# Optimization experiments

Hardware: AMD Instinct MI355X
Metric: run time of the kernel (lower is better)

The kernel has to match this reference:

```python
import jax, jax.numpy as jnp
import numpy as np

KEEP_P = 0.75  # 1 - dropout_p, dropout_p = 0.25

def setup_inputs() -> dict:
    key = jax.random.key(0)
    k1, k2, k3, k4 = jax.random.split(key, 4)
    B, Sq, Skv, D, Dv = 8, 2048, 2048, 128, 128
    x1 = jax.random.normal(k1, (B, Sq, D), dtype=jnp.float32)
    x2 = jax.random.normal(k2, (B, Skv, D), dtype=jnp.float32)
    x3 = jax.random.normal(k3, (B, Skv, Dv), dtype=jnp.float32)
    # torch Dropout(p): mask = bernoulli(keep_p) / keep_p
    keep = jax.random.bernoulli(k4, KEEP_P, (B, Sq, Skv))
    dropout_mask = keep.astype(jnp.float32) / KEEP_P
    return {"x1": x1, "x2": x2, "x3": x3, "dropout_mask": dropout_mask}

def reference(x1, x2, x3, dropout_mask):
    # scores: [B, Sq, Skv] = x1 @ x2^T (no scale: scale_factor is None)
    scores = jnp.einsum("bqd,bkd->bqk", x1, x2)
    probs = jax.nn.softmax(scores, axis=-1)
    probs = probs * dropout_mask  # dropout with fixed mask
    out = jnp.einsum("bqk,bkv->bqv", probs, x3)  # [B, Sq, Dv]
    return out
```

## Files before the change

### kernel.cpp

```cpp
#include <hip/hip_runtime.h>
#include <stdint.h>

#define SQ 2048
#define SKV 2048
#define DD 128
#define NB 8
#define M0 40.0f
#define KEEP_INV 1.3333333333333333f

typedef float  f4v  __attribute__((ext_vector_type(4)));
typedef __bf16 bf4  __attribute__((ext_vector_type(4)));
typedef __bf16 bf8  __attribute__((ext_vector_type(8)));

__device__ __forceinline__ void async16(const void* g, void* l) {
    __builtin_amdgcn_global_load_lds(
        (const __attribute__((address_space(1))) void*)g,
        (__attribute__((address_space(3))) void*)l, 16, 0, 0);
}

__device__ __forceinline__ f4v mfma16(bf8 a, bf8 b, f4v c) {
    return __builtin_amdgcn_mfma_f32_16x16x32_bf16(a, b, c, 0, 0, 0);
}

__global__ void cast_hilo_swz(const float* __restrict__ src,
                              __bf16* __restrict__ hi, __bf16* __restrict__ lo) {
    int tid = blockIdx.x * 256 + threadIdx.x;
    int d8 = tid & 15;
    int kv = (tid >> 4) & (SKV - 1);
    int b  = tid >> 15;
    const float* p = src + ((size_t)b * SKV + kv) * DD + d8 * 8;
    f4v a0 = *(const f4v*)p;
    f4v a1 = *(const f4v*)(p + 4);
    bf8 h, l;
#pragma unroll
    for (int c = 0; c < 4; c++) {
        __bf16 h0 = (__bf16)a0[c]; __bf16 h1 = (__bf16)a1[c];
        h[c] = h0; h[c + 4] = h1;
        l[c]     = (__bf16)(a0[c] - (float)h0);
        l[c + 4] = (__bf16)(a1[c] - (float)h1);
    }
    int s = d8 >> 2, g = d8 & 3, kb32 = kv >> 5, row = kv & 31;
    size_t off = (size_t)(b * 64 + kb32) * 4096 + (size_t)((s * 32 + row) * 4 + g) * 8;
    *(bf8*)(hi + off) = h;
    *(bf8*)(lo + off) = l;
}

__global__ void transpose_v_swz(const float* __restrict__ v, __bf16* __restrict__ vtf) {
    __shared__ __bf16 tile[32][33];
    int kb32 = blockIdx.x, dv0 = blockIdx.y * 32, b = blockIdx.z;
    int tx = threadIdx.x, ty = threadIdx.y;
    const float* src = v + ((size_t)b * SKV + kb32 * 32 + ty) * DD + dv0 + tx;
#pragma unroll
    for (int i = 0; i < 32; i += 8)
        tile[ty + i][tx] = (__bf16)src[(size_t)i * DD];
    __syncthreads();
    int pcol = (tx < 16) ? ((tx >> 2) << 3) + (tx & 3)
                         : (((tx - 16) >> 2) << 3) + 4 + (tx & 3);
    __bf16* dst = vtf + (size_t)(b * 64 + kb32) * 4096 + pcol;
#pragma unroll
    for (int i = 0; i < 32; i += 8)
        dst[(size_t)(dv0 + ty + i) * 32] = tile[tx][ty + i];
}

__global__ void maskbits_kernel(const float* __restrict__ mask,
                                uint32_t* __restrict__ bits) {
    int tid = blockIdx.x * 256 + threadIdx.x;
    const f4v* m = (const f4v*)(mask + (size_t)tid * 32);
    uint32_t w = 0;
#pragma unroll
    for (int c = 0; c < 8; c++) {
        f4v x = m[c];
        w |= (x.x > 0.5f ? 1u : 0u) << (c * 4);
        w |= (x.y > 0.5f ? 1u : 0u) << (c * 4 + 1);
        w |= (x.z > 0.5f ? 1u : 0u) << (c * 4 + 2);
        w |= (x.w > 0.5f ? 1u : 0u) << (c * 4 + 3);
    }
    bits[tid] = w;
}

__global__ __launch_bounds__(256, 3) void attn_kernel(
    const float* __restrict__ Qf, const __bf16* __restrict__ KV,
    const uint32_t* __restrict__ Mbits, __bf16* __restrict__ O_part,
    float* __restrict__ l_part, int nsp, int kv_len) {
    __shared__ __bf16 lds[2][12288];
    const int lin = blockIdx.x;
    const int per_xcd = (NB * nsp) >> 3;
    const int xcd = lin & 7;
    const int idx = lin >> 3;
    const int slice = xcd * per_xcd + (idx >> 5);
    const int qblk = idx & 31;
    const int b = slice / nsp, sid = slice % nsp;
    const int tid = threadIdx.x;
    const int w = tid >> 6, lane = tid & 63;
    const int g = lane >> 4, n = lane & 15;
    const int qb = qblk * 64 + w * 16;
    const int kb32_0 = (sid * kv_len) >> 5;
    const int niter = kv_len >> 5;
    const size_t kelems = (size_t)NB * SKV * DD;

    const float* Qrow = Qf + ((size_t)b * SQ + qb + n) * DD + g * 8;
    bf8 qh[4], ql[4];
#pragma unroll
    for (int s = 0; s < 4; s++) {
        f4v v0 = *(const f4v*)(Qrow + s * 32);
        f4v v1 = *(const f4v*)(Qrow + s * 32 + 4);
#pragma unroll
        for (int c = 0; c < 4; c++) {
            __bf16 h0 = (__bf16)v0[c];
            __bf16 h1 = (__bf16)v1[c];
            qh[s][c]     = h0;
            qh[s][c + 4] = h1;
            ql[s][c]     = (__bf16)(v0[c] - (float)h0);
            ql[s][c + 4] = (__bf16)(v1[c] - (float)h1);
        }
    }

    const __bf16* gblk0 = KV + (size_t)(b * 64 + kb32_0) * 4096;
    auto stage = [&](int buf, int it) {
        const __bf16* gb = gblk0 + (size_t)it * 4096;
#pragma unroll
        for (int jj = 0; jj < 6; jj++) {
            int j = w * 6 + jj;
            int arr = j >> 3, sub = j & 7;
            async16(gb + (size_t)arr * kelems + sub * 512 + lane * 8,
                    (void*)&lds[buf][arr * 4096 + sub * 512]);
        }
    };

    const uint32_t* Mrow = Mbits + ((size_t)b * SQ + qb + n) * (SKV / 32) + kb32_0;
    stage(0, 0);
    uint32_t mw_c = Mrow[0];
    uint32_t mw_n = (niter > 1) ? Mrow[1] : mw_c;

    const f4v zero = {0.f, 0.f, 0.f, 0.f};
    f4v o_acc[8];
#pragma unroll
    for (int t = 0; t < 8; t++) o_acc[t] = zero;
    float l_run = 0.f;

    for (int it = 0; it < niter; it++) {
        __syncthreads();
        if (it + 1 < niter) stage((it + 1) & 1, it + 1);
        uint32_t mw_p = Mrow[(it + 2 < niter) ? it + 2 : niter - 1];

        const __bf16* L = lds[it & 1];
        f4v sa0 = zero, sa1 = zero;
#pragma unroll
        for (int s = 0; s < 4; s++) {
            bf8 ah0 = *(const bf8*)(L + (size_t)((s * 32 + n) * 4 + g) * 8);
            bf8 ah1 = *(const bf8*)(L + (size_t)((s * 32 + n + 16) * 4 + g) * 8);
            bf8 al0 = *(const bf8*)(L + 4096 + (size_t)((s * 32 + n) * 4 + g) * 8);
            bf8 al1 = *(const bf8*)(L + 4096 + (size_t)((s * 32 + n + 16) * 4 + g) * 8);
            sa0 = mfma16(ah0, qh[s], sa0);
            sa1 = mfma16(ah1, qh[s], sa1);
            sa0 = mfma16(ah0, ql[s], sa0);
            sa1 = mfma16(ah1, ql[s], sa1);
            sa0 = mfma16(al0, qh[s], sa0);
            sa1 = mfma16(al1, qh[s], sa1);
        }

        float p0e[4], p1e[4];
#pragma unroll
        for (int r = 0; r < 4; r++) {
            p0e[r] = __expf(sa0[r] - M0);
            p1e[r] = __expf(sa1[r] - M0);
            l_run += p0e[r] + p1e[r];
        }
        bf8 pf;
#pragma unroll
        for (int j = 0; j < 4; j++) {
            pf[j]     = ((mw_c >> (4 * g + j)) & 1)      ? (__bf16)p0e[j] : (__bf16)0.0f;
            pf[j + 4] = ((mw_c >> (16 + 4 * g + j)) & 1) ? (__bf16)p1e[j] : (__bf16)0.0f;
        }
#pragma unroll
        for (int t = 0; t < 8; t++) {
            bf8 vf = *(const bf8*)(L + 8192 + (size_t)((t * 16 + n) * 4 + g) * 8);
            o_acc[t] = mfma16(pf, vf, o_acc[t]);
        }
        mw_c = mw_n; mw_n = mw_p;
    }

    l_run += __shfl_xor(l_run, 16);
    l_run += __shfl_xor(l_run, 32);
    const int tile = (b * 128 + qblk * 4 + w) * nsp + sid;
    __bf16* op = O_part + (size_t)tile * 2048;
#pragma unroll
    for (int t = 0; t < 8; t++)
#pragma unroll
        for (int r = 0; r < 4; r++)
            op[(g * 4 + r) * 128 + t * 16 + n] = (__bf16)o_acc[t][r];
    if (g == 0) l_part[(size_t)tile * 16 + n] = l_run;
}

__global__ __launch_bounds__(256) void combine_kernel(
    const __bf16* __restrict__ O_part, const float* __restrict__ l_part,
    float* __restrict__ out, int nsp) {
    const int qt = blockIdx.x;
    const int b  = blockIdx.y;
    const int tbase = (b * 128 + qt) * nsp;
    const int q  = threadIdx.x >> 4;
    const int d8 = threadIdx.x & 15;
    float acc[8] = {0.f, 0.f, 0.f, 0.f, 0.f, 0.f, 0.f, 0.f};
    float L = 0.f;
    for (int s = 0; s < nsp; s++) {
        const __bf16* op = O_part + (size_t)(tbase + s) * 2048 + q * 128 + d8 * 8;
        bf4 v0 = *(const bf4*)op;
        bf4 v1 = *(const bf4*)(op + 4);
#pragma unroll
        for (int e = 0; e < 4; e++) {
            acc[e]     += (float)v0[e];
            acc[e + 4] += (float)v1[e];
        }
        L += l_part[(size_t)(tbase + s) * 16 + q];
    }
    float scale = KEEP_INV / L;
    f4v w0, w1;
#pragma unroll
    for (int e = 0; e < 4; e++) { w0[e] = acc[e] * scale; w1[e] = acc[e + 4] * scale; }
    float* o = out + ((size_t)b * SQ + qt * 16 + q) * DD + d8 * 8;
    *(f4v*)o = w0;
    *(f4v*)(o + 4) = w1;
}

extern "C" void kernel_launch(void* const* d_in, const int* in_sizes, int n_in,
                              void* d_out, int out_size, void* d_ws, size_t ws_size,
                              hipStream_t stream) {
    const float* x1   = (const float*)d_in[0];
    const float* x2   = (const float*)d_in[1];
    const float* x3   = (const float*)d_in[2];
    const float* mask = (const float*)d_in[3];
    float* out = (float*)d_out;

    const size_t kelems = (size_t)NB * SKV * DD;
    __bf16*   Khif = (__bf16*)d_ws;
    __bf16*   Klof = Khif + kelems;
    __bf16*   VTf  = Klof + kelems;
    uint32_t* Mb   = (uint32_t*)(VTf + kelems);
    const size_t mwords = (size_t)NB * SQ * (SKV / 32);
    __bf16*   O_part = (__bf16*)(Mb + mwords);

    size_t base = 3 * kelems * sizeof(__bf16) + mwords * 4;
    size_t per  = (size_t)NB * 128 * (2048 * sizeof(__bf16) + 16 * 4);
    int nsp = 4;
    while (nsp > 1 && base + (size_t)nsp * per > ws_size) nsp >>= 1;
    float* l_part = (float*)(O_part + (size_t)NB * 128 * nsp * 2048);

    hipLaunchKernelGGL(cast_hilo_swz, dim3(NB * SKV * 16 / 256), dim3(256), 0, stream,
                       x2, Khif, Klof);
    hipLaunchKernelGGL(transpose_v_swz, dim3(SKV / 32, DD / 32, NB), dim3(32, 8), 0,
                       stream, x3, VTf);
    hipLaunchKernelGGL(maskbits_kernel, dim3(NB * SQ * 64 / 256), dim3(256), 0, stream,
                       mask, Mb);
    hipLaunchKernelGGL(attn_kernel, dim3(32 * NB * nsp), dim3(256), 0, stream,
                       x1, Khif, Mb, O_part, l_part, nsp, SKV / nsp);
    hipLaunchKernelGGL(combine_kernel, dim3(128, NB), dim3(256), 0, stream,
                       O_part, l_part, out, nsp);
}
```

Measured before the change: 264.9 us.

## Replace split-bf16 QK^T with single fp16 MFMA and fp32 partials

Drops the hi/lo bf16 split of Q and K, which cost three MFMAs per tile, in favour of a single fp16 cast and one f16 MFMA per tile. This cuts QK matrix work by three times and removes the K-low staging, shrinking LDS per stage and raising the occupancy hint to 4. Partial outputs are now stored in fp32 instead of bf16, adding write and read traffic in the combine step. The risk is accuracy: scores from unscaled dot products with D=128 may lose precision or overflow in fp16, while exp uses a fixed M0 offset.

```diff
diff --git a/kernel.cpp b/kernel.cpp
--- a/kernel.cpp
+++ b/kernel.cpp
@@ -8,9 +8,10 @@
 #define M0 40.0f
 #define KEEP_INV 1.3333333333333333f
 
-typedef float  f4v  __attribute__((ext_vector_type(4)));
-typedef __bf16 bf4  __attribute__((ext_vector_type(4)));
-typedef __bf16 bf8  __attribute__((ext_vector_type(8)));
+typedef float    f4v __attribute__((ext_vector_type(4)));
+typedef __bf16   bf4 __attribute__((ext_vector_type(4)));
+typedef __bf16   bf8 __attribute__((ext_vector_type(8)));
+typedef _Float16 h8  __attribute__((ext_vector_type(8)));
 
 __device__ __forceinline__ void async16(const void* g, void* l) {
     __builtin_amdgcn_global_load_lds(
@@ -18,12 +19,8 @@
         (__attribute__((address_space(3))) void*)l, 16, 0, 0);
 }
 
-__device__ __forceinline__ f4v mfma16(bf8 a, bf8 b, f4v c) {
-    return __builtin_amdgcn_mfma_f32_16x16x32_bf16(a, b, c, 0, 0, 0);
-}
-
-__global__ void cast_hilo_swz(const float* __restrict__ src,
-                              __bf16* __restrict__ hi, __bf16* __restrict__ lo) {
+__global__ void cast_f16_swz(const float* __restrict__ src,
+                             _Float16* __restrict__ dst) {
     int tid = blockIdx.x * 256 + threadIdx.x;
     int d8 = tid & 15;
     int kv = (tid >> 4) & (SKV - 1);
@@ -31,18 +28,14 @@
     const float* p = src + ((size_t)b * SKV + kv) * DD + d8 * 8;
     f4v a0 = *(const f4v*)p;
     f4v a1 = *(const f4v*)(p + 4);
-    bf8 h, l;
+    h8 h;
 #pragma unroll
     for (int c = 0; c < 4; c++) {
-        __bf16 h0 = (__bf16)a0[c]; __bf16 h1 = (__bf16)a1[c];
-        h[c] = h0; h[c + 4] = h1;
-        l[c]     = (__bf16)(a0[c] - (float)h0);
-        l[c + 4] = (__bf16)(a1[c] - (float)h1);
+        h[c]     = (_Float16)a0[c];
+        h[c + 4] = (_Float16)a1[c];
     }
     int s = d8 >> 2, g = d8 & 3, kb32 = kv >> 5, row = kv & 31;
-    size_t off = (size_t)(b * 64 + kb32) * 4096 + (size_t)((s * 32 + row) * 4 + g) * 8;
-    *(bf8*)(hi + off) = h;
-    *(bf8*)(lo + off) = l;
+    *(h8*)(dst + (size_t)(b * 64 + kb32) * 4096 + (size_t)((s * 32 + row) * 4 + g) * 8) = h;
 }
 
 __global__ void transpose_v_swz(const float* __restrict__ v, __bf16* __restrict__ vtf) {
@@ -78,11 +71,12 @@
     bits[tid] = w;
 }
 
-__global__ __launch_bounds__(256, 3) void attn_kernel(
-    const float* __restrict__ Qf, const __bf16* __restrict__ KV,
-    const uint32_t* __restrict__ Mbits, __bf16* __restrict__ O_part,
-    float* __restrict__ l_part, int nsp, int kv_len) {
-    __shared__ __bf16 lds[2][12288];
+__global__ __launch_bounds__(256, 4) void attn_kernel(
+    const float* __restrict__ Qf, const _Float16* __restrict__ Kh,
+    const __bf16* __restrict__ Vt, const uint32_t* __restrict__ Mbits,
+    float* __restrict__ O_part, float* __restrict__ l_part,
+    int nsp, int kv_len) {
+    __shared__ __align__(16) char smem[2][16384];
     const int lin = blockIdx.x;
     const int per_xcd = (NB * nsp) >> 3;
     const int xcd = lin & 7;
@@ -96,34 +90,32 @@
     const int qb = qblk * 64 + w * 16;
     const int kb32_0 = (sid * kv_len) >> 5;
     const int niter = kv_len >> 5;
-    const size_t kelems = (size_t)NB * SKV * DD;
 
     const float* Qrow = Qf + ((size_t)b * SQ + qb + n) * DD + g * 8;
-    bf8 qh[4], ql[4];
+    h8 qf[4];
 #pragma unroll
     for (int s = 0; s < 4; s++) {
         f4v v0 = *(const f4v*)(Qrow + s * 32);
         f4v v1 = *(const f4v*)(Qrow + s * 32 + 4);
 #pragma unroll
         for (int c = 0; c < 4; c++) {
-            __bf16 h0 = (__bf16)v0[c];
-            __bf16 h1 = (__bf16)v1[c];
-            qh[s][c]     = h0;
-            qh[s][c + 4] = h1;
-            ql[s][c]     = (__bf16)(v0[c] - (float)h0);
-            ql[s][c + 4] = (__bf16)(v1[c] - (float)h1);
-        }
-    }
-
-    const __bf16* gblk0 = KV + (size_t)(b * 64 + kb32_0) * 4096;
+            qf[s][c]     = (_Float16)v0[c];
+            qf[s][c + 4] = (_Float16)v1[c];
+        }
+    }
+
+    const _Float16* Kt0 = Kh + (size_t)(b * 64 + kb32_0) * 4096;
+    const __bf16*   Vt0 = Vt + (size_t)(b * 64 + kb32_0) * 4096;
     auto stage = [&](int buf, int it) {
-        const __bf16* gb = gblk0 + (size_t)it * 4096;
-#pragma unroll
-        for (int jj = 0; jj < 6; jj++) {
-            int j = w * 6 + jj;
-            int arr = j >> 3, sub = j & 7;
-            async16(gb + (size_t)arr * kelems + sub * 512 + lane * 8,
-                    (void*)&lds[buf][arr * 4096 + sub * 512]);
+#pragma unroll
+        for (int jj = 0; jj < 4; jj++) {
+            int j = w * 4 + jj;
+            if (j < 8)
+                async16(Kt0 + (size_t)it * 4096 + j * 512 + lane * 8,
+                        (void*)&smem[buf][j * 1024]);
+            else
+                async16(Vt0 + (size_t)it * 4096 + (j - 8) * 512 + lane * 8,
+                        (void*)&smem[buf][8192 + (j - 8) * 1024]);
         }
     };
 
@@ -143,20 +135,16 @@
         if (it + 1 < niter) stage((it + 1) & 1, it + 1);
         uint32_t mw_p = Mrow[(it + 2 < niter) ? it + 2 : niter - 1];
 
-        const __bf16* L = lds[it & 1];
+        const _Float16* Lk = (const _Float16*)smem[it & 1];
+        const __bf16*   Lv = (const __bf16*)(smem[it & 1] + 8192);
+
         f4v sa0 = zero, sa1 = zero;
 #pragma unroll
         for (int s = 0; s < 4; s++) {
-            bf8 ah0 = *(const bf8*)(L + (size_t)((s * 32 + n) * 4 + g) * 8);
-            bf8 ah1 = *(const bf8*)(L + (size_t)((s * 32 + n + 16) * 4 + g) * 8);
-            bf8 al0 = *(const bf8*)(L + 4096 + (size_t)((s * 32 + n) * 4 + g) * 8);
-            bf8 al1 = *(const bf8*)(L + 4096 + (size_t)((s * 32 + n + 16) * 4 + g) * 8);
-            sa0 = mfma16(ah0, qh[s], sa0);
-            sa1 = mfma16(ah1, qh[s], sa1);
-            sa0 = mfma16(ah0, ql[s], sa0);
-            sa1 = mfma16(ah1, ql[s], sa1);
-            sa0 = mfma16(al0, qh[s], sa0);
-            sa1 = mfma16(al1, qh[s], sa1);
+            h8 a0 = *(const h8*)(Lk + (size_t)((s * 32 + n) * 4 + g) * 8);
+            h8 a1 = *(const h8*)(Lk + (size_t)((s * 32 + n + 16) * 4 + g) * 8);
+            sa0 = __builtin_amdgcn_mfma_f32_16x16x32_f16(a0, qf[s], sa0, 0, 0, 0);
+            sa1 = __builtin_amdgcn_mfma_f32_16x16x32_f16(a1, qf[s], sa1, 0, 0, 0);
         }
 
         float p0e[4], p1e[4];
@@ -172,10 +160,11 @@
             pf[j]     = ((mw_c >> (4 * g + j)) & 1)      ? (__bf16)p0e[j] : (__bf16)0.0f;
             pf[j + 4] = ((mw_c >> (16 + 4 * g + j)) & 1) ? (__bf16)p1e[j] : (__bf16)0.0f;
         }
+
 #pragma unroll
         for (int t = 0; t < 8; t++) {
-            bf8 vf = *(const bf8*)(L + 8192 + (size_t)((t * 16 + n) * 4 + g) * 8);
-            o_acc[t] = mfma16(pf, vf, o_acc[t]);
+            bf8 vf = *(const bf8*)(Lv + (size_t)((t * 16 + n) * 4 + g) * 8);
+            o_acc[t] = __builtin_amdgcn_mfma_f32_16x16x32_bf16(pf, vf, o_acc[t], 0, 0, 0);
         }
         mw_c = mw_n; mw_n = mw_p;
     }
@@ -183,43 +172,35 @@
     l_run += __shfl_xor(l_run, 16);
     l_run += __shfl_xor(l_run, 32);
     const int tile = (b * 128 + qblk * 4 + w) * nsp + sid;
-    __bf16* op = O_part + (size_t)tile * 2048;
+    float* op = O_part + (size_t)tile * 2048;
 #pragma unroll
     for (int t = 0; t < 8; t++)
 #pragma unroll
         for (int r = 0; r < 4; r++)
-            op[(g * 4 + r) * 128 + t * 16 + n] = (__bf16)o_acc[t][r];
+            op[(g * 4 + r) * 128 + t * 16 + n] = o_acc[t][r];
     if (g == 0) l_part[(size_t)tile * 16 + n] = l_run;
 }
 
 __global__ __launch_bounds__(256) void combine_kernel(
-    const __bf16* __restrict__ O_part, const float* __restrict__ l_part,
+    const float* __restrict__ O_part, const float* __restrict__ l_part,
     float* __restrict__ out, int nsp) {
     const int qt = blockIdx.x;
     const int b  = blockIdx.y;
     const int tbase = (b * 128 + qt) * nsp;
     const int q  = threadIdx.x >> 4;
     const int d8 = threadIdx.x & 15;
-    float acc[8] = {0.f, 0.f, 0.f, 0.f, 0.f, 0.f, 0.f, 0.f};
+    f4v a0 = {0.f, 0.f, 0.f, 0.f}, a1 = {0.f, 0.f, 0.f, 0.f};
     float L = 0.f;
     for (int s = 0; s < nsp; s++) {
-        const __bf16* op = O_part + (size_t)(tbase + s) * 2048 + q * 128 + d8 * 8;
-        bf4 v0 = *(const bf4*)op;
-        bf4 v1 = *(const bf4*)(op + 4);
-#pragma unroll
-        for (int e = 0; e < 4; e++) {
-            acc[e]     += (float)v0[e];
-            acc[e + 4] += (float)v1[e];
-        }
-        L += l_part[(size_t)(tbase + s) * 16 + q];
+        const float* op = O_part + (size_t)(tbase + s) * 2048 + q * 128 + d8 * 8;
+        a0 += *(const f4v*)op;
+        a1 += *(const f4v*)(op + 4);
+        L  += l_part[(size_t)(tbase + s) * 16 + q];
     }
     float scale = KEEP_INV / L;
-    f4v w0, w1;
-#pragma unroll
-    for (int e = 0; e < 4; e++) { w0[e] = acc[e] * scale; w1[e] = acc[e + 4] * scale; }
     float* o = out + ((size_t)b * SQ + qt * 16 + q) * DD + d8 * 8;
-    *(f4v*)o = w0;
-    *(f4v*)(o + 4) = w1;
+    *(f4v*)o       = a0 * scale;
+    *(f4v*)(o + 4) = a1 * scale;
 }
 
 extern "C" void kernel_launch(void* const* d_in, const int* in_sizes, int n_in,
@@ -232,27 +213,26 @@
     float* out = (float*)d_out;
 
     const size_t kelems = (size_t)NB * SKV * DD;
-    __bf16*   Khif = (__bf16*)d_ws;
-    __bf16*   Klof = Khif + kelems;
-    __bf16*   VTf  = Klof + kelems;
-    uint32_t* Mb   = (uint32_t*)(VTf + kelems);
+    _Float16* Kh  = (_Float16*)d_ws;
+    __bf16*   VTf = (__bf16*)(Kh + kelems);
+    uint32_t* Mb  = (uint32_t*)(VTf + kelems);
     const size_t mwords = (size_t)NB * SQ * (SKV / 32);
-    __bf16*   O_part = (__bf16*)(Mb + mwords);
-
-    size_t base = 3 * kelems * sizeof(__bf16) + mwords * 4;
-    size_t per  = (size_t)NB * 128 * (2048 * sizeof(__bf16) + 16 * 4);
+    float*    O_part = (float*)(Mb + mwords);
+
+    size_t base = 2 * kelems * 2 + mwords * 4;
+    size_t per  = (size_t)NB * 128 * (2048 + 16) * sizeof(float);
     int nsp = 4;
     while (nsp > 1 && base + (size_t)nsp * per > ws_size) nsp >>= 1;
-    float* l_part = (float*)(O_part + (size_t)NB * 128 * nsp * 2048);
-
-    hipLaunchKernelGGL(cast_hilo_swz, dim3(NB * SKV * 16 / 256), dim3(256), 0, stream,
-                       x2, Khif, Klof);
+    float* l_part = O_part + (size_t)NB * 128 * nsp * 2048;
+
+    hipLaunchKernelGGL(cast_f16_swz, dim3(NB * SKV * 16 / 256), dim3(256), 0, stream,
+                       x2, Kh);
     hipLaunchKernelGGL(transpose_v_swz, dim3(SKV / 32, DD / 32, NB), dim3(32, 8), 0,
                        stream, x3, VTf);
     hipLaunchKernelGGL(maskbits_kernel, dim3(NB * SQ * 64 / 256), dim3(256), 0, stream,
                        mask, Mb);
     hipLaunchKernelGGL(attn_kernel, dim3(32 * NB * nsp), dim3(256), 0, stream,
-                       x1, Khif, Mb, O_part, l_part, nsp, SKV / nsp);
+                       x1, Kh, VTf, Mb, O_part, l_part, nsp, SKV / nsp);
     hipLaunchKernelGGL(combine_kernel, dim3(128, NB), dim3(256), 0, stream,
                        O_part, l_part, out, nsp);
 }
```

New measurement: 251.8 us. 4.9% less time.
